# Kernel optimization log

Hardware: AMD Instinct MI355X
Metric: run time of the kernel (lower is better)

## Reference

```python
import jax, jax.numpy as jnp
import numpy as np

BN_EPS = 1e-5

def _resize_hw(x, hw):
    # bilinear per temporal slice (align_corners=False == jax half-pixel 'linear');
    # T dim keeps its size so linear resize is identity along it.
    B, C, T, H, W = x.shape
    return jax.image.resize(x, (B, C, T, hw, hw), method='linear')

def setup_inputs() -> dict:
    key = jax.random.key(0)
    ks = jax.random.split(key, 12)
    Cin, Cmid = 80, 40
    s = lambda k, shp, scale=0.05: jax.random.normal(k, shp, dtype=jnp.float32) * scale
    return {
        'fast': jax.random.normal(ks[0], (1, Cin, 4, 64, 64), dtype=jnp.float32),
        'slow': jax.random.normal(ks[1], (1, Cin, 4, 64, 64), dtype=jnp.float32),
        'g_w': s(ks[2], (Cmid, Cin)), 'g_b': s(ks[3], (Cmid,)),
        'th_w': s(ks[4], (Cmid, Cin)), 'th_b': s(ks[5], (Cmid,)),
        'ph_w': s(ks[6], (Cmid, Cin)), 'ph_b': s(ks[7], (Cmid,)),
        'wz_w': s(ks[8], (Cin, Cmid)), 'wz_b': s(ks[9], (Cin,)),
        'bn_g': 1.0 + s(ks[10], (Cin,)), 'bn_b': s(ks[11], (Cin,)),
    }

def reference(fast, slow, g_w, g_b, th_w, th_b, ph_w, ph_b, wz_w, wz_b, bn_g, bn_b):
    x_fast = _resize_hw(fast, 32)   # [B,80,4,32,32]
    x_slow = _resize_hw(slow, 32)
    B, C, T, H, W = x_fast.shape
    N = T * H * W
    flat = x_fast.reshape(B, C, N)                      # [B,C,N]
    # 1x1 conv projections (channel contractions)
    g_x = jnp.einsum('oc,bcn->bno', g_w, flat) + g_b          # [B,N,Cm]
    theta = jnp.einsum('oc,bcn->bno', th_w, flat) + th_b      # [B,N,Cm]
    phi = jnp.einsum('oc,bcn->bon', ph_w, flat) + ph_b[None, :, None]  # [B,Cm,N]
    f = jnp.einsum('bnc,bcm->bnm', theta, phi)          # [B,N,N] full attention scores
    f_div_C = jax.nn.softmax(f, axis=-1)                # 'embedded' mode
    y = jnp.einsum('bnm,bmc->bnc', f_div_C, g_x)        # [B,N,Cm]
    y = y.transpose(0, 2, 1).reshape(B, -1, T, H, W)    # [B,Cm,T,H,W]
    # W_z: 1x1 conv then training-mode BatchNorm3d (batch stats over N,T,H,W)
    wy = jnp.einsum('oc,bcthw->bothw', wz_w, y) + wz_b[None, :, None, None, None]
    mean = jnp.mean(wy, axis=(0, 2, 3, 4), keepdims=True)
    var = jnp.var(wy, axis=(0, 2, 3, 4), keepdims=True)
    gamma = bn_g[None, :, None, None, None]
    beta = bn_b[None, :, None, None, None]
    wy = (wy - mean) * jax.lax.rsqrt(var + BN_EPS) * gamma + beta
    z = wy * x_slow                                     # elementwise fast/slow fusion
    return _resize_hw(z, 64)                            # [B,80,4,64,64]
```

## Files before the change

kernel.cpp:

```cpp
#include <hip/hip_runtime.h>

typedef unsigned int u32;
typedef __bf16 bf16x8 __attribute__((ext_vector_type(8)));
typedef float f32x4 __attribute__((ext_vector_type(4)));
typedef u32 u32x4 __attribute__((ext_vector_type(4)));


static __device__ __forceinline__ u32 f2bf(float f) {
    u32 u = __float_as_uint(f);
    return (u + 0x7fffu + ((u >> 16) & 1u)) >> 16;
}

__device__ __forceinline__ void taps_down(int i, int* j, float* w) {
    if (i == 0) {
        j[0]=0; j[1]=0; j[2]=1; j[3]=2;
        w[0]=0.f; w[1]=3.f/7.f; w[2]=3.f/7.f; w[3]=1.f/7.f;
    } else if (i == 31) {
        j[0]=61; j[1]=62; j[2]=63; j[3]=63;
        w[0]=1.f/7.f; w[1]=3.f/7.f; w[2]=3.f/7.f; w[3]=0.f;
    } else {
        j[0]=2*i-1; j[1]=2*i; j[2]=2*i+1; j[3]=2*i+2;
        w[0]=0.125f; w[1]=0.375f; w[2]=0.375f; w[3]=0.125f;
    }
}

__global__ __launch_bounds__(256) void k_down(
        const float* __restrict__ fast, const float* __restrict__ slow,
        float* __restrict__ xf, float* __restrict__ xs) {
    int idx = blockIdx.x * 256 + threadIdx.x;
    int which = idx >= 327680;
    int rem = which ? idx - 327680 : idx;
    const float* src = which ? slow : fast;
    float* dst = which ? xs : xf;
    int c = rem >> 12;
    int n = rem & 4095;
    int tt = n >> 10, hh = (n >> 5) & 31, ww = n & 31;
    int jy[4], jx[4]; float wy[4], wx[4];
    taps_down(hh, jy, wy);
    taps_down(ww, jx, wx);
    const float* base = src + ((c * 4 + tt) << 12);
    float acc = 0.f;
#pragma unroll
    for (int a = 0; a < 4; ++a) {
        const float* row = base + (jy[a] << 6);
        acc += wy[a] * (wx[0]*row[jx[0]] + wx[1]*row[jx[1]]
                      + wx[2]*row[jx[2]] + wx[3]*row[jx[3]]);
    }
    dst[rem] = acc;
}

__global__ __launch_bounds__(256) void k_proj(
        const float* __restrict__ xf,
        const float* __restrict__ gw, const float* __restrict__ gb,
        const float* __restrict__ thw, const float* __restrict__ thb,
        const float* __restrict__ phw, const float* __restrict__ phb,
        unsigned short* __restrict__ gxP, unsigned short* __restrict__ thetaP,
        unsigned short* __restrict__ phiP) {
    __shared__ float sW[960];
    __shared__ float sB[12];
    int t = threadIdx.x;
    int o0 = blockIdx.y * 4;
    for (int i = t; i < 960; i += 256) {
        int mat = i / 320, rem = i % 320;
        int oo = rem / 80, c = rem % 80;
        const float* w = (mat == 0) ? gw : ((mat == 1) ? thw : phw);
        sW[i] = w[(o0 + oo) * 80 + c];
    }
    if (t < 12) {
        int mat = t / 4, oo = t % 4;
        const float* b = (mat == 0) ? gb : ((mat == 1) ? thb : phb);
        sB[t] = b[o0 + oo];
    }
    __syncthreads();
    int n = blockIdx.x * 256 + t;
    if (blockIdx.y == 0) {
#pragma unroll
        for (int c = 40; c < 64; ++c) { thetaP[n*64 + c] = 0; phiP[n*64 + c] = 0; }
#pragma unroll
        for (int r = 40; r < 48; ++r) gxP[r * 4096 + n] = 0;
    }
    float x[80];
#pragma unroll
    for (int c = 0; c < 80; ++c) x[c] = xf[c * 4096 + n];
#pragma unroll
    for (int mat = 0; mat < 3; ++mat) {
#pragma unroll
        for (int oo = 0; oo < 4; ++oo) {
            float acc = sB[mat * 4 + oo];
            const float4* w4 = (const float4*)&sW[mat * 320 + oo * 80];
#pragma unroll
            for (int cq = 0; cq < 20; ++cq) {
                float4 w = w4[cq];
                acc += w.x * x[cq*4] + w.y * x[cq*4+1] + w.z * x[cq*4+2] + w.w * x[cq*4+3];
            }
            int o = o0 + oo;
            if (mat == 0)      gxP[o * 4096 + n]  = (unsigned short)f2bf(acc);
            else if (mat == 1) thetaP[n * 64 + o] = (unsigned short)f2bf(acc);
            else               phiP[n * 64 + o]   = (unsigned short)f2bf(acc);
        }
    }
}

#define YMM(acc, gfr, bfr) \
    acc = __builtin_amdgcn_mfma_f32_16x16x32_bf16( \
        __builtin_bit_cast(bf16x8, gfr), __builtin_bit_cast(bf16x8, bfr), acc, 0, 0, 0)

__global__ __launch_bounds__(256) void k_attn(
        const unsigned short* __restrict__ thetaP,
        const unsigned short* __restrict__ phiP,
        const unsigned short* __restrict__ gxP,
        float* __restrict__ ypart, float* __restrict__ spart) {
    int lane = threadIdx.x & 63;
    int wv = threadIdx.x >> 6;
    int n0 = blockIdx.x * 64 + wv * 16;
    int ck = blockIdx.y;
    int nl = lane & 15, q = lane >> 4;

    const unsigned short* thp = thetaP + (n0 + nl) * 64 + q * 8;
    u32x4 tb0 = *(const u32x4*)(thp);
    u32x4 tb1 = *(const u32x4*)(thp + 32);

    f32x4 y0 = {0.f,0.f,0.f,0.f}, y1 = y0, y2 = y0;
    float ssum = 0.f;
    int idx0 = ((((q & 1) << 5) + nl) << 2);
    int idx1 = idx0 + 64;

    u32x4 pfA[4], pfB[4], gfA[3], gfB[3];
    int mbase = ck * 512;

#define LOADBLK(P, G, BLK) do {                                              \
        int m0_ = mbase + (BLK) * 32;                                        \
        const unsigned short* pp0_ = phiP + (m0_ + nl) * 64 + q * 8;         \
        const unsigned short* pp1_ = phiP + (m0_ + 16 + nl) * 64 + q * 8;    \
        P[0] = *(const u32x4*)pp0_;  P[1] = *(const u32x4*)(pp0_ + 32);      \
        P[2] = *(const u32x4*)pp1_;  P[3] = *(const u32x4*)(pp1_ + 32);      \
        G[0] = *(const u32x4*)(gxP + (nl) * 4096      + m0_ + q * 8);        \
        G[1] = *(const u32x4*)(gxP + (16 + nl) * 4096 + m0_ + q * 8);        \
        G[2] = *(const u32x4*)(gxP + (32 + nl) * 4096 + m0_ + q * 8);        \
    } while (0)

#define COMPUTE(P, G) do {                                                   \
        u32 p0[2], p1[2];                                                    \
        _Pragma("unroll")                                                    \
        for (int Tm = 0; Tm < 2; ++Tm) {                                     \
            f32x4 f = {0.f,0.f,0.f,0.f};                                     \
            f = __builtin_amdgcn_mfma_f32_16x16x32_bf16(                     \
                __builtin_bit_cast(bf16x8, P[Tm*2+0]),                       \
                __builtin_bit_cast(bf16x8, tb0), f, 0, 0, 0);                \
            f = __builtin_amdgcn_mfma_f32_16x16x32_bf16(                     \
                __builtin_bit_cast(bf16x8, P[Tm*2+1]),                       \
                __builtin_bit_cast(bf16x8, tb1), f, 0, 0, 0);                \
            float e0 = __expf(f[0]), e1 = __expf(f[1]);                      \
            float e2 = __expf(f[2]), e3 = __expf(f[3]);                      \
            ssum += (e0 + e1) + (e2 + e3);                                   \
            p0[Tm] = f2bf(e0) | (f2bf(e1) << 16);                            \
            p1[Tm] = f2bf(e2) | (f2bf(e3) << 16);                            \
        }                                                                    \
        int a0 = __builtin_amdgcn_ds_bpermute(idx0, (int)p0[0]);             \
        int a1 = __builtin_amdgcn_ds_bpermute(idx0, (int)p1[0]);             \
        int a2 = __builtin_amdgcn_ds_bpermute(idx1, (int)p0[0]);             \
        int a3 = __builtin_amdgcn_ds_bpermute(idx1, (int)p1[0]);             \
        int b0 = __builtin_amdgcn_ds_bpermute(idx0, (int)p0[1]);             \
        int b1 = __builtin_amdgcn_ds_bpermute(idx0, (int)p1[1]);             \
        int b2 = __builtin_amdgcn_ds_bpermute(idx1, (int)p0[1]);             \
        int b3 = __builtin_amdgcn_ds_bpermute(idx1, (int)p1[1]);             \
        u32x4 bf_;                                                           \
        bf_[0] = (u32)(q < 2 ? a0 : b0);  bf_[1] = (u32)(q < 2 ? a1 : b1);   \
        bf_[2] = (u32)(q < 2 ? a2 : b2);  bf_[3] = (u32)(q < 2 ? a3 : b3);   \
        YMM(y0, G[0], bf_);  YMM(y1, G[1], bf_);  YMM(y2, G[2], bf_);        \
    } while (0)

    LOADBLK(pfA, gfA, 0);
#pragma unroll 1
    for (int bb = 0; bb < 8; ++bb) {
        LOADBLK(pfB, gfB, bb * 2 + 1);
        COMPUTE(pfA, gfA);
        if (bb < 7) LOADBLK(pfA, gfA, bb * 2 + 2);
        COMPUTE(pfB, gfB);
    }

    ssum += __shfl_xor(ssum, 16);
    ssum += __shfl_xor(ssum, 32);
    if (q == 0) spart[ck * 4096 + n0 + nl] = ssum;

    float* yp = ypart + (size_t)ck * 48 * 4096 + n0 + nl;
#pragma unroll
    for (int r = 0; r < 4; ++r) yp[(q * 4 + r) * 4096] = y0[r];
#pragma unroll
    for (int r = 0; r < 4; ++r) yp[(16 + q * 4 + r) * 4096] = y1[r];
#pragma unroll
    for (int r = 0; r < 4; ++r) yp[(32 + q * 4 + r) * 4096] = y2[r];
}

__global__ __launch_bounds__(256) void k_combine(
        const float* __restrict__ ypart, const float* __restrict__ spart,
        float* __restrict__ yfin) {
    int idx = blockIdx.x * 256 + threadIdx.x;
    int o = idx >> 10;
    int n4 = (idx & 1023) * 4;
    float4 sv[8];
#pragma unroll
    for (int ck = 0; ck < 8; ++ck)
        sv[ck] = *(const float4*)(spart + ck * 4096 + n4);
    float4 yv[8];
#pragma unroll
    for (int ck = 0; ck < 8; ++ck)
        yv[ck] = *(const float4*)(ypart + (size_t)(ck * 48 + o) * 4096 + n4);
    float4 ss = make_float4(0.f,0.f,0.f,0.f), acc = ss;
#pragma unroll
    for (int ck = 0; ck < 8; ++ck) {
        ss.x += sv[ck].x; ss.y += sv[ck].y; ss.z += sv[ck].z; ss.w += sv[ck].w;
        acc.x += yv[ck].x; acc.y += yv[ck].y; acc.z += yv[ck].z; acc.w += yv[ck].w;
    }
    float4 r = make_float4(acc.x/ss.x, acc.y/ss.y, acc.z/ss.z, acc.w/ss.w);
    *(float4*)(yfin + o * 4096 + n4) = r;
}

__device__ __forceinline__ void taps_up(int i, int* j0, int* j1, float* w0, float* w1) {
    if (i == 0)        { *j0 = 0;        *j1 = 0;          *w0 = 0.f;   *w1 = 1.f;   }
    else if (i == 63)  { *j0 = 31;       *j1 = 31;         *w0 = 1.f;   *w1 = 0.f;   }
    else if (i & 1)    { *j0 = i >> 1;   *j1 = (i>>1) + 1; *w0 = 0.75f; *w1 = 0.25f; }
    else               { *j0 = (i>>1)-1; *j1 = i >> 1;     *w0 = 0.25f; *w1 = 0.75f; }
}

__global__ __launch_bounds__(256) void k_bn_up(
        const float* __restrict__ yfin, const float* __restrict__ wzw,
        const float* __restrict__ wzb, const float* __restrict__ bng,
        const float* __restrict__ bnb, const float* __restrict__ xs,
        float* __restrict__ out) {
    __shared__ float4 wrow4[1024];
    __shared__ float sred[8];
    int ch = blockIdx.x;
    int t = threadIdx.x;
    float w[40];
#pragma unroll
    for (int o = 0; o < 40; ++o) w[o] = wzw[ch * 40 + o];
    float bias = wzb[ch];
    float s1 = 0.f, s2 = 0.f;
#pragma unroll 1
    for (int k = 0; k < 4; ++k) {
        int i = k * 256 + t;
        float4 yv[40];
#pragma unroll
        for (int o = 0; o < 40; ++o)
            yv[o] = *(const float4*)(yfin + o * 4096 + i * 4);
        float4 a = make_float4(bias, bias, bias, bias);
#pragma unroll
        for (int o = 0; o < 40; ++o) {
            a.x += w[o]*yv[o].x; a.y += w[o]*yv[o].y;
            a.z += w[o]*yv[o].z; a.w += w[o]*yv[o].w;
        }
        wrow4[i] = a;
        s1 += a.x + a.y + a.z + a.w;
        s2 += a.x*a.x + a.y*a.y + a.z*a.z + a.w*a.w;
    }
#pragma unroll
    for (int off = 32; off > 0; off >>= 1) {
        s1 += __shfl_down(s1, off);
        s2 += __shfl_down(s2, off);
    }
    int wid = t >> 6;
    if ((t & 63) == 0) { sred[wid] = s1; sred[4 + wid] = s2; }
    __syncthreads();
    float mean = (sred[0] + sred[1] + sred[2] + sred[3]) * (1.f / 4096.f);
    float var  = (sred[4] + sred[5] + sred[6] + sred[7]) * (1.f / 4096.f) - mean * mean;
    float inv = rsqrtf(var + 1e-5f);
    float sc = bng[ch] * inv;
    float sh = bnb[ch] - mean * sc;
#pragma unroll
    for (int k = 0; k < 4; ++k) {
        int i = k * 256 + t;
        float4 a = wrow4[i];
        float4 xv = *(const float4*)(xs + ch * 4096 + i * 4);
        a.x = (a.x*sc + sh)*xv.x; a.y = (a.y*sc + sh)*xv.y;
        a.z = (a.z*sc + sh)*xv.z; a.w = (a.w*sc + sh)*xv.w;
        wrow4[i] = a;
    }
    __syncthreads();
    const float* zs = (const float*)wrow4;
    int chbase = ch << 14;
#pragma unroll 4
    for (int k = 0; k < 64; ++k) {
        int p = k * 256 + t;
        int tt = p >> 12, yy = (p >> 6) & 63, xx = p & 63;
        int jy0, jy1, jx0, jx1; float wy0, wy1, wx0, wx1;
        taps_up(yy, &jy0, &jy1, &wy0, &wy1);
        taps_up(xx, &jx0, &jx1, &wx0, &wx1);
        const float* pl = zs + tt * 1024;
        float r0 = wx0*pl[jy0*32 + jx0] + wx1*pl[jy0*32 + jx1];
        float r1 = wx0*pl[jy1*32 + jx0] + wx1*pl[jy1*32 + jx1];
        out[chbase + p] = wy0*r0 + wy1*r1;
    }
}

extern "C" void kernel_launch(void* const* d_in, const int* in_sizes, int n_in,
                              void* d_out, int out_size, void* d_ws, size_t ws_size,
                              hipStream_t stream) {
    const float* fast = (const float*)d_in[0];
    const float* slow = (const float*)d_in[1];
    const float* g_w  = (const float*)d_in[2];
    const float* g_b  = (const float*)d_in[3];
    const float* th_w = (const float*)d_in[4];
    const float* th_b = (const float*)d_in[5];
    const float* ph_w = (const float*)d_in[6];
    const float* ph_b = (const float*)d_in[7];
    const float* wz_w = (const float*)d_in[8];
    const float* wz_b = (const float*)d_in[9];
    const float* bn_g = (const float*)d_in[10];
    const float* bn_b = (const float*)d_in[11];
    float* out = (float*)d_out;
    float* ws  = (float*)d_ws;

    float* xf = ws;
    float* xs = ws + 327680;
    unsigned short* thetaP = (unsigned short*)(ws + 655360);
    unsigned short* phiP   = (unsigned short*)(ws + 786432);
    unsigned short* gxP    = (unsigned short*)(ws + 917504);
    float* ypart = ws + 1015808;
    float* spart = ws + 2588672;
    float* yfin  = ws + 2621440;

    k_down<<<2560, 256, 0, stream>>>(fast, slow, xf, xs);
    k_proj<<<dim3(16, 10), 256, 0, stream>>>(xf, g_w, g_b, th_w, th_b, ph_w, ph_b,
                                             gxP, thetaP, phiP);
    k_attn<<<dim3(64, 8), 256, 0, stream>>>(thetaP, phiP, gxP, ypart, spart);
    k_combine<<<160, 256, 0, stream>>>(ypart, spart, yfin);
    k_bn_up<<<80, 256, 0, stream>>>(yfin, wz_w, wz_b, bn_g, bn_b, xs, out);
}
```

Measured before the change: 147.4 us.

## Fuse bilinear downsample into projection kernel, recomputing taps per block

Merges the downsample and 1x1-projection kernels into one launch. Each projection block recomputes the fast-input bilinear downsample directly into registers, so the intermediate xf buffer is never written or read. An extra row of blocks downsamples the slow input and zeroes the padding. This saves a kernel launch and a global round trip, but the fast downsample is now computed redundantly by all ten output-channel groups and the slow path runs with few threads.

```diff
diff --git a/kernel.cpp b/kernel.cpp
--- a/kernel.cpp
+++ b/kernel.cpp
@@ -24,42 +24,44 @@
     }
 }
 
-__global__ __launch_bounds__(256) void k_down(
+__global__ __launch_bounds__(256) void k_dp(
         const float* __restrict__ fast, const float* __restrict__ slow,
-        float* __restrict__ xf, float* __restrict__ xs) {
-    int idx = blockIdx.x * 256 + threadIdx.x;
-    int which = idx >= 327680;
-    int rem = which ? idx - 327680 : idx;
-    const float* src = which ? slow : fast;
-    float* dst = which ? xs : xf;
-    int c = rem >> 12;
-    int n = rem & 4095;
+        const float* __restrict__ gw, const float* __restrict__ gb,
+        const float* __restrict__ thw, const float* __restrict__ thb,
+        const float* __restrict__ phw, const float* __restrict__ phb,
+        unsigned short* __restrict__ gxP, unsigned short* __restrict__ thetaP,
+        unsigned short* __restrict__ phiP, float* __restrict__ xs) {
+    __shared__ float sW[960];
+    __shared__ float sB[12];
+    int t = threadIdx.x;
+    int by = blockIdx.y;
+    int n = blockIdx.x * 256 + t;
     int tt = n >> 10, hh = (n >> 5) & 31, ww = n & 31;
     int jy[4], jx[4]; float wy[4], wx[4];
     taps_down(hh, jy, wy);
     taps_down(ww, jx, wx);
-    const float* base = src + ((c * 4 + tt) << 12);
-    float acc = 0.f;
-#pragma unroll
-    for (int a = 0; a < 4; ++a) {
-        const float* row = base + (jy[a] << 6);
-        acc += wy[a] * (wx[0]*row[jx[0]] + wx[1]*row[jx[1]]
-                      + wx[2]*row[jx[2]] + wx[3]*row[jx[3]]);
-    }
-    dst[rem] = acc;
-}
-
-__global__ __launch_bounds__(256) void k_proj(
-        const float* __restrict__ xf,
-        const float* __restrict__ gw, const float* __restrict__ gb,
-        const float* __restrict__ thw, const float* __restrict__ thb,
-        const float* __restrict__ phw, const float* __restrict__ phb,
-        unsigned short* __restrict__ gxP, unsigned short* __restrict__ thetaP,
-        unsigned short* __restrict__ phiP) {
-    __shared__ float sW[960];
-    __shared__ float sB[12];
-    int t = threadIdx.x;
-    int o0 = blockIdx.y * 4;
+
+    if (by == 10) {
+#pragma unroll 4
+        for (int c = 0; c < 80; ++c) {
+            const float* base = slow + ((c * 4 + tt) << 12);
+            float acc = 0.f;
+#pragma unroll
+            for (int a = 0; a < 4; ++a) {
+                const float* row = base + (jy[a] << 6);
+                acc += wy[a] * (wx[0]*row[jx[0]] + wx[1]*row[jx[1]]
+                              + wx[2]*row[jx[2]] + wx[3]*row[jx[3]]);
+            }
+            xs[c * 4096 + n] = acc;
+        }
+#pragma unroll
+        for (int c = 40; c < 64; ++c) { thetaP[n*64 + c] = 0; phiP[n*64 + c] = 0; }
+#pragma unroll
+        for (int r = 40; r < 48; ++r) gxP[r * 4096 + n] = 0;
+        return;
+    }
+
+    int o0 = by * 4;
     for (int i = t; i < 960; i += 256) {
         int mat = i / 320, rem = i % 320;
         int oo = rem / 80, c = rem % 80;
@@ -72,16 +74,20 @@
         sB[t] = b[o0 + oo];
     }
     __syncthreads();
-    int n = blockIdx.x * 256 + t;
-    if (blockIdx.y == 0) {
-#pragma unroll
-        for (int c = 40; c < 64; ++c) { thetaP[n*64 + c] = 0; phiP[n*64 + c] = 0; }
-#pragma unroll
-        for (int r = 40; r < 48; ++r) gxP[r * 4096 + n] = 0;
-    }
+
     float x[80];
-#pragma unroll
-    for (int c = 0; c < 80; ++c) x[c] = xf[c * 4096 + n];
+#pragma unroll 8
+    for (int c = 0; c < 80; ++c) {
+        const float* base = fast + ((c * 4 + tt) << 12);
+        float acc = 0.f;
+#pragma unroll
+        for (int a = 0; a < 4; ++a) {
+            const float* row = base + (jy[a] << 6);
+            acc += wy[a] * (wx[0]*row[jx[0]] + wx[1]*row[jx[1]]
+                          + wx[2]*row[jx[2]] + wx[3]*row[jx[3]]);
+        }
+        x[c] = acc;
+    }
 #pragma unroll
     for (int mat = 0; mat < 3; ++mat) {
 #pragma unroll
@@ -311,7 +317,6 @@
     float* out = (float*)d_out;
     float* ws  = (float*)d_ws;
 
-    float* xf = ws;
     float* xs = ws + 327680;
     unsigned short* thetaP = (unsigned short*)(ws + 655360);
     unsigned short* phiP   = (unsigned short*)(ws + 786432);
@@ -320,9 +325,8 @@
     float* spart = ws + 2588672;
     float* yfin  = ws + 2621440;
 
-    k_down<<<2560, 256, 0, stream>>>(fast, slow, xf, xs);
-    k_proj<<<dim3(16, 10), 256, 0, stream>>>(xf, g_w, g_b, th_w, th_b, ph_w, ph_b,
-                                             gxP, thetaP, phiP);
+    k_dp<<<dim3(16, 11), 256, 0, stream>>>(fast, slow, g_w, g_b, th_w, th_b,
+                                           ph_w, ph_b, gxP, thetaP, phiP, xs);
     k_attn<<<dim3(64, 8), 256, 0, stream>>>(thetaP, phiP, gxP, ypart, spart);
     k_combine<<<160, 256, 0, stream>>>(ypart, spart, yfin);
     k_bn_up<<<80, 256, 0, stream>>>(yfin, wz_w, wz_b, bn_g, bn_b, xs, out);
```

New measurement: 222.4 us. 1.51x slower.
